# Performance work log

Hardware: AMD Instinct MI355X
Metric: run time of the kernel (lower is better)

Reference implementation:

```python
import jax, jax.numpy as jnp
import numpy as np

B, T, N, F_, KH, D, KD = 16, 12, 325, 64, 4, 16, 3  # batch, time, nodes, feat, heads, head_dim, diffusion steps
H = KH // 2
EPS = 1e-5


def setup_inputs() -> dict:
    key = jax.random.key(0)
    ks = jax.random.split(key, 16)
    lin = lambda k: (jax.random.normal(k, (F_, F_), jnp.float32) * 0.02)
    return {
        "x": jax.random.normal(ks[0], (B, T, N, F_), jnp.float32),
        "A": jax.random.uniform(ks[1], (KD, N, N), jnp.float32),
        "AT": jax.random.uniform(ks[2], (KD, N, N), jnp.float32),
        "Wq": lin(ks[3]), "bq": jnp.zeros((F_,), jnp.float32),
        "Wk": lin(ks[4]), "bk": jnp.zeros((F_,), jnp.float32),
        "Wks": lin(ks[5]), "bks": jnp.zeros((F_,), jnp.float32),
        "Wv": lin(ks[6]), "bv": jnp.zeros((F_,), jnp.float32),
        "Wvs": lin(ks[7]), "bvs": jnp.zeros((F_,), jnp.float32),
        "Wdi": jax.random.normal(ks[8], (H, KD, N, N), jnp.float32) * 0.05,
        "Wdo": jax.random.normal(ks[9], (H, KD, N, N), jnp.float32) * 0.05,
        "Wf1": lin(ks[10]), "bf1": jnp.zeros((F_,), jnp.float32),
        "Wf2": lin(ks[11]), "bf2": jnp.zeros((F_,), jnp.float32),
        "g_ln": jnp.ones((F_,), jnp.float32), "b_ln": jnp.zeros((F_,), jnp.float32),
    }


def _heads(y):
    # [B,T,N,F] -> [KH,B,T,N,D]  (torch.split along -1 then stack on dim 0)
    return y.reshape(B, T, N, KH, D).transpose(3, 0, 1, 2, 4)


def _attn_half(q, k, ks_, v, vs, bias):
    # q,k,ks_,v,vs: [H,B,T,N,D]; bias: [H,1,1,N,N]
    scale = 1.0 / jnp.sqrt(jnp.float32(D))
    e = jnp.einsum('hbtnd,hbtmd->hbtnm', q, k) * scale + bias
    es = jax.nn.sigmoid((q * ks_).sum(-1, keepdims=True) * scale)  # [H,B,T,N,1]
    e = e - e.max(-1, keepdims=True)
    ex = jnp.exp(e)
    a = ex / (es + ex.sum(-1, keepdims=True))  # sigmoid-augmented softmax
    out = jnp.einsum('hbtnm,hbtmd->hbtnd', a, v)
    return out + vs - a.sum(-1, keepdims=True) * vs


def reference(x, A, AT, Wq, bq, Wk, bk, Wks, bks, Wv, bv, Wvs, bvs,
              Wdi, Wdo, Wf1, bf1, Wf2, bf2, g_ln, b_ln):
    q = _heads(x @ Wq.T + bq)
    k = _heads(x @ Wk.T + bk)
    ks_ = _heads(x @ Wks.T + bks)
    v = _heads(x @ Wv.T + bv)
    vs = _heads(x @ Wvs.T + bvs)

    # DCN graph-diffusion bias: sum_j W[h,j] * A[j] -> [H,1,1,N,N]
    bias_i = jnp.einsum('hknm,knm->hnm', Wdi, A)[:, None, None]
    bias_o = jnp.einsum('hknm,knm->hnm', Wdo, AT)[:, None, None]

    vi = _attn_half(q[:H], k[:H], ks_[:H], v[:H], vs[:H], bias_i)
    vo = _attn_half(q[H:], k[H:], ks_[H:], v[H:], vs[H:], bias_o)

    val = jnp.concatenate([vi, vo], 0)  # [KH,B,T,N,D]
    val = val.transpose(1, 2, 3, 0, 4).reshape(B, T, N, F_)

    h = jax.nn.gelu(val @ Wf1.T + bf1, approximate=False) @ Wf2.T + bf2
    h = h + x

    mu = h.mean(-1, keepdims=True)
    var = ((h - mu) ** 2).mean(-1, keepdims=True)
    return g_ln * (h - mu) / jnp.sqrt(var + EPS) + b_ln
```

## Files before the change

kernel.cpp:

```cpp
#include <hip/hip_runtime.h>
#include <hip/hip_bf16.h>
#include <math.h>

#define NN 325
#define FD 64
#define KH 4
#define DH 16
#define BT 192
#define NN2 (NN*NN)
#define PST (NN*DH)
#define WSL 5632
#define HSTR 72
#define NPROJ 975
#define NBIAS 1848
#define NPAD  (KH*BT)
#define ANB   2112
#define LOG2E 1.44269504088896f

typedef __attribute__((ext_vector_type(8))) short short8;
typedef __attribute__((ext_vector_type(4))) float f32x4;

union U8 { uint4 u; short8 s; ushort us[8]; };
__device__ inline short8 lds8(const ushort* p){ U8 t; t.u = *(const uint4*)p; return t.s; }
__device__ inline float b2f(ushort v){ return __uint_as_float(((unsigned)v) << 16); }
__device__ inline ushort f2b(float f){
  unsigned u = __float_as_uint(f);
  u += 0x7fff + ((u >> 16) & 1);
  return (ushort)(u >> 16);
}
__device__ inline unsigned pk2(float a, float b){
  union { __hip_bfloat162 h; unsigned u; } t;
  t.h = __float22bfloat162_rn(float2{a, b});
  return t.u;
}
__device__ inline short8 cvt8(const float* p){
  float4 u = ((const float4*)p)[0], v = ((const float4*)p)[1];
  U8 t;
  t.us[0]=f2b(u.x); t.us[1]=f2b(u.y); t.us[2]=f2b(u.z); t.us[3]=f2b(u.w);
  t.us[4]=f2b(v.x); t.us[5]=f2b(v.y); t.us[6]=f2b(v.z); t.us[7]=f2b(v.w);
  return t.s;
}

__global__ __launch_bounds__(256) void wpack_kernel(
    const float* __restrict__ Wq,  const float* __restrict__ bq,
    const float* __restrict__ Wk,  const float* __restrict__ bk,
    const float* __restrict__ Wks, const float* __restrict__ bks,
    const float* __restrict__ Wv,  const float* __restrict__ bv,
    const float* __restrict__ Wvs, const float* __restrict__ bvs,
    const float* __restrict__ Wf1, const float* __restrict__ Wf2,
    ushort* __restrict__ Wcat, float* __restrict__ bcat){
  int blk = blockIdx.x;
  const float* Ws[7] = {Wq, Wk, Wks, Wv, Wvs, Wf1, Wf2};
  const float* bs[5] = {bq, bk, bks, bv, bvs};
  int f = blk * 64 + (threadIdx.x >> 2);
  int c0 = (threadIdx.x & 3) * 8;
  const float* wr = Ws[blk] + (f & 63) * 64;
  unsigned* dst = (unsigned*)Wcat + f * 32 + c0;
  #pragma unroll
  for (int c = 0; c < 8; ++c)
    dst[c] = f2b(wr[2*(c0+c)]) | ((unsigned)f2b(wr[2*(c0+c)+1]) << 16);
  if (blk < 5 && (threadIdx.x & 3) == 0) bcat[f] = bs[blk][f & 63];
}

__global__ __launch_bounds__(256) void prep_kernel(
    const float* __restrict__ x, const ushort* __restrict__ Wcat,
    const float* __restrict__ bcat, ushort* __restrict__ proj,
    ushort* __restrict__ vt, ushort* __restrict__ kperm,
    const float* __restrict__ Wdi, const float* __restrict__ Wdo,
    const float* __restrict__ A,   const float* __restrict__ AT,
    float* __restrict__ biasF){
  int bid = blockIdx.x, tid = threadIdx.x;
  if (bid < NPROJ){
    int lane = tid & 63, wid = tid >> 6;
    int r0 = bid * 64 + wid * 16;
    int m = lane & 15, g = lane >> 4;
    int gr = r0 + m;
    int bt = gr / NN, n = gr - bt * NN;
    const float* xr = x + (size_t)gr * 64 + g * 8;
    short8 xb0 = cvt8(xr);
    short8 xb1 = cvt8(xr + 32);
    for (int ct = 0; ct < 20; ++ct){
      short8 w0 = lds8(Wcat + ((size_t)(ct*16 + m) * 64 + g * 8));
      short8 w1 = lds8(Wcat + ((size_t)(ct*16 + m) * 64 + g * 8 + 32));
      float4 b4 = *(const float4*)(bcat + ct*16 + 4*g);
      f32x4 acc = {b4.x, b4.y, b4.z, b4.w};
      acc = __builtin_amdgcn_mfma_f32_16x16x32_bf16(w0, xb0, acc, 0, 0, 0);
      acc = __builtin_amdgcn_mfma_f32_16x16x32_bf16(w1, xb1, acc, 0, 0, 0);
      if (ct >= 4 && ct < 8){
        int w = n & 31;
        ushort* kd = kperm + (size_t)((ct-4)*BT + bt) * WSL
                   + (n >> 5)*512 + ((w >> 2) & 1)*256
                   + (4*(w >> 3) + (w & 3))*16 + 4*g;
        uint2 wv; wv.x = pk2(acc[0], acc[1]); wv.y = pk2(acc[2], acc[3]);
        *(uint2*)kd = wv;
      } else if (ct >= 12 && ct < 16){
        ushort* vs = vt + (size_t)((ct-12)*BT + bt) * WSL + (n >> 5)*512 + (n & 31);
        #pragma unroll
        for (int rg = 0; rg < 4; ++rg)
          vs[(4*g + rg) * 32] = f2b(acc[rg]);
      } else {
        int slot = (ct < 4) ? ct : (ct < 12 ? ct - 4 : ct - 8);
        float sc = (ct < 4) ? 0.25f * LOG2E : 1.0f;
        uint2 w2;
        w2.x = pk2(acc[0]*sc, acc[1]*sc);
        w2.y = pk2(acc[2]*sc, acc[3]*sc);
        *(uint2*)(proj + ((size_t)slot * BT + bt) * PST + n*16 + 4*g) = w2;
      }
    }
  } else if (bid < NPROJ + NBIAS){
    int idx = (bid - NPROJ) * 256 + tid;
    int h = idx / 118272;
    int rem = idx - h * 118272;
    int qt = rem / 5632;
    int r2 = rem - qt * 5632;
    int tt = r2 >> 9, r3 = r2 & 511;
    int gg = r3 >> 7, mm = (r3 >> 3) & 15, e8 = r3 & 7;
    int n = qt*16 + mm;
    int tok = tt*32 + gg*8 + e8;
    float s = -1e30f;
    if (n < NN && tok < NN){
      int ridx = n * NN + tok;
      s = 0.f;
      if (h < 2){
        #pragma unroll
        for (int k = 0; k < 3; ++k) s += Wdi[(h*3 + k)*NN2 + ridx] * A[k*NN2 + ridx];
      } else {
        int h2 = h - 2;
        #pragma unroll
        for (int k = 0; k < 3; ++k) s += Wdo[(h2*3 + k)*NN2 + ridx] * AT[k*NN2 + ridx];
      }
      s *= LOG2E;
    }
    biasF[idx] = s;
  } else {
    int slice = bid - NPROJ - NBIAS;
    if (tid < 432){
      int d = tid / 27, wz = 5 + tid % 27;
      vt[(size_t)slice * WSL + 5120 + d*32 + wz] = 0;
      int half = (wz >> 2) & 1, rr = 4*(wz >> 3) + (wz & 3);
      kperm[(size_t)slice * WSL + 5120 + half*256 + rr*16 + d] = 0;
    }
  }
}

__global__ __launch_bounds__(256, 3) void attn_kernel(
    const ushort* __restrict__ proj, const float* __restrict__ biasF,
    const ushort* __restrict__ vt, const ushort* __restrict__ kperm,
    ushort* __restrict__ val){
  int tid = threadIdx.x, lane = tid & 63, wid = tid >> 6;
  int bid = (int)blockIdx.x;
  int swz = (bid & 7) * (ANB/8) + (bid >> 3);
  int p = swz * 4 + wid;
  int j = p % 11, bh = p / 11;
  int h = bh / BT, bt = bh - h * BT;
  int qt1 = 2*j;
  int two = (j < 10);
  int qt2 = two ? qt1 + 1 : qt1;
  int m = lane & 15, g = lane >> 4;

  const ushort* qb  = proj + (size_t)((0*KH + h)*BT + bt) * PST;
  const ushort* ksb = proj + (size_t)((1*KH + h)*BT + bt) * PST;
  const ushort* vsb = proj + (size_t)((2*KH + h)*BT + bt) * PST;
  const ushort* ka  = kperm + (size_t)(h*BT + bt) * WSL + m*16 + (g&1)*8;
  const ushort* va  = vt    + (size_t)(h*BT + bt) * WSL + m*32 + g*8;
  const float*  b1a = biasF + (size_t)(h*21 + qt1) * WSL + g*128 + m*8;
  const float*  b2a = biasF + (size_t)(h*21 + qt2) * WSL + g*128 + m*8;

  short8 zero = {0,0,0,0,0,0,0,0};
  short8 qf1 = (g < 2) ? lds8(qb + (size_t)(qt1*16 + m)*16 + (g&1)*8) : zero;
  short8 qf2 = (g < 2) ? lds8(qb + (size_t)(qt2*16 + m)*16 + (g&1)*8) : zero;

  int nb1 = min(qt1*16 + m, NN-1), nb2 = min(qt2*16 + m, NN-1);
  uint2 qw1 = *(const uint2*)(qb  + (size_t)nb1*16 + g*4);
  uint2 kw1 = *(const uint2*)(ksb + (size_t)nb1*16 + g*4);
  uint2 qw2 = *(const uint2*)(qb  + (size_t)nb2*16 + g*4);
  uint2 kw2 = *(const uint2*)(ksb + (size_t)nb2*16 + g*4);

  short8 kE = lds8(ka), kO = lds8(ka + 256), vv = lds8(va);
  f32x4 bE1 = *(const f32x4*)(b1a), bO1 = *(const f32x4*)(b1a + 4);
  f32x4 bE2 = *(const f32x4*)(b2a), bO2 = *(const f32x4*)(b2a + 4);

  short8 ones = {16256,16256,16256,16256,16256,16256,16256,16256};
  f32x4 o1 = {0.f,0.f,0.f,0.f}, o2 = {0.f,0.f,0.f,0.f};
  f32x4 r1 = {0.f,0.f,0.f,0.f}, r2 = {0.f,0.f,0.f,0.f};

  #pragma unroll
  for (int tt = 0; tt < 11; ++tt){
    short8 kEn = zero, kOn = zero, vvn = zero;
    f32x4 bE1n = bE1, bO1n = bO1, bE2n = bE2, bO2n = bO2;
    if (tt < 10){
      const ushort* kan = ka + (tt+1)*512;
      kEn  = lds8(kan); kOn = lds8(kan + 256);
      vvn  = lds8(va + (tt+1)*512);
      bE1n = *(const f32x4*)(b1a + (tt+1)*512);
      bO1n = *(const f32x4*)(b1a + (tt+1)*512 + 4);
      bE2n = *(const f32x4*)(b2a + (tt+1)*512);
      bO2n = *(const f32x4*)(b2a + (tt+1)*512 + 4);
    }
    f32x4 aE1 = __builtin_amdgcn_mfma_f32_16x16x32_bf16(kE, qf1, bE1, 0, 0, 0);
    f32x4 aO1 = __builtin_amdgcn_mfma_f32_16x16x32_bf16(kO, qf1, bO1, 0, 0, 0);
    float e0 = __builtin_amdgcn_exp2f(aE1[0]);
    float e1 = __builtin_amdgcn_exp2f(aE1[1]);
    float e2 = __builtin_amdgcn_exp2f(aE1[2]);
    float e3 = __builtin_amdgcn_exp2f(aE1[3]);
    float e4 = __builtin_amdgcn_exp2f(aO1[0]);
    float e5 = __builtin_amdgcn_exp2f(aO1[1]);
    float e6 = __builtin_amdgcn_exp2f(aO1[2]);
    float e7 = __builtin_amdgcn_exp2f(aO1[3]);
    U8 p1;
    p1.u.x = pk2(e0, e1); p1.u.y = pk2(e2, e3);
    p1.u.z = pk2(e4, e5); p1.u.w = pk2(e6, e7);
    o1 = __builtin_amdgcn_mfma_f32_16x16x32_bf16(p1.s, vv,   o1, 0, 0, 0);
    r1 = __builtin_amdgcn_mfma_f32_16x16x32_bf16(p1.s, ones, r1, 0, 0, 0);
    f32x4 aE2 = __builtin_amdgcn_mfma_f32_16x16x32_bf16(kE, qf2, bE2, 0, 0, 0);
    f32x4 aO2 = __builtin_amdgcn_mfma_f32_16x16x32_bf16(kO, qf2, bO2, 0, 0, 0);
    float f0 = __builtin_amdgcn_exp2f(aE2[0]);
    float f1 = __builtin_amdgcn_exp2f(aE2[1]);
    float f2 = __builtin_amdgcn_exp2f(aE2[2]);
    float f3 = __builtin_amdgcn_exp2f(aE2[3]);
    float f4 = __builtin_amdgcn_exp2f(aO2[0]);
    float f5 = __builtin_amdgcn_exp2f(aO2[1]);
    float f6 = __builtin_amdgcn_exp2f(aO2[2]);
    float f7 = __builtin_amdgcn_exp2f(aO2[3]);
    U8 p2;
    p2.u.x = pk2(f0, f1); p2.u.y = pk2(f2, f3);
    p2.u.z = pk2(f4, f5); p2.u.w = pk2(f6, f7);
    o2 = __builtin_amdgcn_mfma_f32_16x16x32_bf16(p2.s, vv,   o2, 0, 0, 0);
    r2 = __builtin_amdgcn_mfma_f32_16x16x32_bf16(p2.s, ones, r2, 0, 0, 0);
    kE = kEn; kO = kOn; vv = vvn;
    bE1 = bE1n; bO1 = bO1n; bE2 = bE2n; bO2 = bO2n;
  }

  float dp1 = b2f((ushort)(qw1.x & 0xffff)) * b2f((ushort)(kw1.x & 0xffff))
            + b2f((ushort)(qw1.x >> 16))    * b2f((ushort)(kw1.x >> 16))
            + b2f((ushort)(qw1.y & 0xffff)) * b2f((ushort)(kw1.y & 0xffff))
            + b2f((ushort)(qw1.y >> 16))    * b2f((ushort)(kw1.y >> 16));
  float dp2 = b2f((ushort)(qw2.x & 0xffff)) * b2f((ushort)(kw2.x & 0xffff))
            + b2f((ushort)(qw2.x >> 16))    * b2f((ushort)(kw2.x >> 16))
            + b2f((ushort)(qw2.y & 0xffff)) * b2f((ushort)(kw2.y & 0xffff))
            + b2f((ushort)(qw2.y >> 16))    * b2f((ushort)(kw2.y >> 16));
  dp1 += __shfl_xor(dp1, 16, 64); dp1 += __shfl_xor(dp1, 32, 64);
  dp2 += __shfl_xor(dp2, 16, 64); dp2 += __shfl_xor(dp2, 32, 64);
  int sb = g << 4;
  #pragma unroll
  for (int rg = 0; rg < 4; ++rg){
    float d1 = __uint_as_float(__builtin_amdgcn_ds_bpermute(sb + rg*4, __float_as_uint(dp1)));
    float d2 = __uint_as_float(__builtin_amdgcn_ds_bpermute(sb + rg*4, __float_as_uint(dp2)));
    float es1 = __builtin_amdgcn_rcpf(1.f + __builtin_amdgcn_exp2f(-d1));
    float es2 = __builtin_amdgcn_rcpf(1.f + __builtin_amdgcn_exp2f(-d2));
    int n1 = qt1*16 + 4*g + rg;
    int n2 = qt2*16 + 4*g + rg;
    float vsx1 = b2f(vsb[(size_t)min(n1, NN-1)*16 + m]);
    float vsx2 = b2f(vsb[(size_t)min(n2, NN-1)*16 + m]);
    float iv1 = __builtin_amdgcn_rcpf(es1 + r1[rg]);
    float res1 = (o1[rg] + es1 * vsx1) * iv1;
    if (n1 < NN) val[((size_t)bt*NN + n1)*FD + h*16 + m] = f2b(res1);
    if (two){
      float iv2 = __builtin_amdgcn_rcpf(es2 + r2[rg]);
      float res2 = (o2[rg] + es2 * vsx2) * iv2;
      if (n2 < NN) val[((size_t)bt*NN + n2)*FD + h*16 + m] = f2b(res2);
    }
  }
}

__global__ __launch_bounds__(256) void ffn_kernel(
    const ushort* __restrict__ val, const float* __restrict__ x,
    const ushort* __restrict__ Wf1b, const float* __restrict__ bf1,
    const ushort* __restrict__ Wf2b, const float* __restrict__ bf2,
    const float* __restrict__ g_ln, const float* __restrict__ b_ln,
    float* __restrict__ out){
  __shared__ ushort hs[4][16 * HSTR];
  int tid = threadIdx.x, lane = tid & 63, wid = tid >> 6;
  int m = lane & 15, g = lane >> 4;
  int r0 = blockIdx.x * 64 + wid * 16;
  int row = r0 + m;

  short8 vb0 = lds8(val + ((size_t)row * 64 + g * 8));
  short8 vb1 = lds8(val + ((size_t)row * 64 + g * 8 + 32));

  #pragma unroll
  for (int ct = 0; ct < 4; ++ct){
    short8 w0 = lds8(Wf1b + ((size_t)(ct*16 + m) * 64 + g * 8));
    short8 w1 = lds8(Wf1b + ((size_t)(ct*16 + m) * 64 + g * 8 + 32));
    float4 b4 = *(const float4*)(bf1 + ct*16 + 4*g);
    f32x4 acc = {b4.x, b4.y, b4.z, b4.w};
    acc = __builtin_amdgcn_mfma_f32_16x16x32_bf16(w0, vb0, acc, 0, 0, 0);
    acc = __builtin_amdgcn_mfma_f32_16x16x32_bf16(w1, vb1, acc, 0, 0, 0);
    uint2 w;
    float g0 = 0.5f*acc[0]*(1.f + erff(acc[0]*0.70710678118654752f));
    float g1 = 0.5f*acc[1]*(1.f + erff(acc[1]*0.70710678118654752f));
    float g2 = 0.5f*acc[2]*(1.f + erff(acc[2]*0.70710678118654752f));
    float g3 = 0.5f*acc[3]*(1.f + erff(acc[3]*0.70710678118654752f));
    w.x = pk2(g0, g1); w.y = pk2(g2, g3);
    *(uint2*)&hs[wid][m * HSTR + ct*16 + 4*g] = w;
  }
  asm volatile("s_waitcnt lgkmcnt(0)" ::: "memory");
  short8 h0 = lds8(&hs[wid][m * HSTR + g * 8]);
  short8 h1 = lds8(&hs[wid][m * HSTR + g * 8 + 32]);

  float t[4][4];
  #pragma unroll
  for (int ct = 0; ct < 4; ++ct){
    short8 w0 = lds8(Wf2b + ((size_t)(ct*16 + m) * 64 + g * 8));
    short8 w1 = lds8(Wf2b + ((size_t)(ct*16 + m) * 64 + g * 8 + 32));
    float4 b4 = *(const float4*)(bf2 + ct*16 + 4*g);
    f32x4 acc = {b4.x, b4.y, b4.z, b4.w};
    acc = __builtin_amdgcn_mfma_f32_16x16x32_bf16(w0, h0, acc, 0, 0, 0);
    acc = __builtin_amdgcn_mfma_f32_16x16x32_bf16(w1, h1, acc, 0, 0, 0);
    float4 xr = *(const float4*)(x + (size_t)row * 64 + ct*16 + 4*g);
    t[ct][0] = acc[0] + xr.x; t[ct][1] = acc[1] + xr.y;
    t[ct][2] = acc[2] + xr.z; t[ct][3] = acc[3] + xr.w;
  }
  float s = 0.f;
  #pragma unroll
  for (int ct = 0; ct < 4; ++ct) s += (t[ct][0]+t[ct][1]) + (t[ct][2]+t[ct][3]);
  s += __shfl_xor(s, 16, 64); s += __shfl_xor(s, 32, 64);
  float mu = s * (1.f/64.f);
  float v = 0.f;
  #pragma unroll
  for (int ct = 0; ct < 4; ++ct){
    #pragma unroll
    for (int rg = 0; rg < 4; ++rg){ float d = t[ct][rg] - mu; v += d*d; }
  }
  v += __shfl_xor(v, 16, 64); v += __shfl_xor(v, 32, 64);
  float rs = rsqrtf(v * (1.f/64.f) + 1e-5f);
  #pragma unroll
  for (int ct = 0; ct < 4; ++ct){
    float4 g4 = *(const float4*)(g_ln + ct*16 + 4*g);
    float4 bb = *(const float4*)(b_ln + ct*16 + 4*g);
    float4 o;
    o.x = g4.x*(t[ct][0]-mu)*rs + bb.x;
    o.y = g4.y*(t[ct][1]-mu)*rs + bb.y;
    o.z = g4.z*(t[ct][2]-mu)*rs + bb.z;
    o.w = g4.w*(t[ct][3]-mu)*rs + bb.w;
    *(float4*)(out + (size_t)row * 64 + ct*16 + 4*g) = o;
  }
}

extern "C" void kernel_launch(void* const* d_in, const int* in_sizes, int n_in,
                              void* d_out, int out_size, void* d_ws, size_t ws_size,
                              hipStream_t stream) {
  const float* x    = (const float*)d_in[0];
  const float* A    = (const float*)d_in[1];
  const float* AT   = (const float*)d_in[2];
  const float* Wq   = (const float*)d_in[3];
  const float* bq   = (const float*)d_in[4];
  const float* Wk   = (const float*)d_in[5];
  const float* bk   = (const float*)d_in[6];
  const float* Wks  = (const float*)d_in[7];
  const float* bks  = (const float*)d_in[8];
  const float* Wv   = (const float*)d_in[9];
  const float* bv   = (const float*)d_in[10];
  const float* Wvs  = (const float*)d_in[11];
  const float* bvs  = (const float*)d_in[12];
  const float* Wdi  = (const float*)d_in[13];
  const float* Wdo  = (const float*)d_in[14];
  const float* Wf1  = (const float*)d_in[15];
  const float* bf1  = (const float*)d_in[16];
  const float* Wf2  = (const float*)d_in[17];
  const float* bf2  = (const float*)d_in[18];
  const float* g_ln = (const float*)d_in[19];
  const float* b_ln = (const float*)d_in[20];
  float* out = (float*)d_out;

  float* ws = (float*)d_ws;
  ushort* proj  = (ushort*)ws;
  float*  biasF = ws + 5990400;
  ushort* val   = (ushort*)(ws + 6463488);
  ushort* vt    = (ushort*)(ws + 8460288);
  ushort* kperm = (ushort*)(ws + 10622976);
  ushort* Wcat  = (ushort*)(ws + 12785664);
  float*  bcat  = ws + 12800000;
  ushort* Wf1b  = Wcat + 320*64;
  ushort* Wf2b  = Wcat + 384*64;

  wpack_kernel<<<7, 256, 0, stream>>>(Wq, bq, Wk, bk, Wks, bks,
                                      Wv, bv, Wvs, bvs, Wf1, Wf2, Wcat, bcat);
  prep_kernel<<<NPROJ + NBIAS + NPAD, 256, 0, stream>>>(
      x, Wcat, bcat, proj, vt, kperm, Wdi, Wdo, A, AT, biasF);
  attn_kernel<<<ANB, 256, 0, stream>>>(proj, biasF, vt, kperm, val);
  ffn_kernel<<<975, 256, 0, stream>>>(val, x, Wf1b, bf1, Wf2b, bf2,
                                      g_ln, b_ln, out);
}
```

Baseline: 188.6 us.

## Stage per-(head,bt) K and V slices in LDS shared across waves

Each attention block now handles one half of the query tiles for a single (head, batch-time) pair. It copies the permuted K and transposed V slices into shared memory once, and all waves then read them from LDS instead of each wave streaming them from global memory. The grid shrinks from 2112 to 1536 blocks and the occupancy hint of 3 blocks per CU is dropped. The costs are an LDS staging step plus a barrier, about 22 KB of LDS per block, and some idle waves: the first half has 6 tiles over 4 waves and the second has 5. The software prefetch of K/V across iterations is also removed.

```diff
diff --git a/kernel.cpp b/kernel.cpp
--- a/kernel.cpp
+++ b/kernel.cpp
@@ -14,7 +14,7 @@
 #define NPROJ 975
 #define NBIAS 1848
 #define NPAD  (KH*BT)
-#define ANB   2112
+#define ANB   1536
 #define LOG2E 1.44269504088896f
 
 typedef __attribute__((ext_vector_type(8))) short short8;
@@ -143,122 +143,137 @@
   }
 }
 
-__global__ __launch_bounds__(256, 3) void attn_kernel(
+__global__ __launch_bounds__(256) void attn_kernel(
     const ushort* __restrict__ proj, const float* __restrict__ biasF,
     const ushort* __restrict__ vt, const ushort* __restrict__ kperm,
     ushort* __restrict__ val){
+  __shared__ __align__(16) ushort Ks[WSL];
+  __shared__ __align__(16) ushort Vs[WSL];
   int tid = threadIdx.x, lane = tid & 63, wid = tid >> 6;
   int bid = (int)blockIdx.x;
-  int swz = (bid & 7) * (ANB/8) + (bid >> 3);
-  int p = swz * 4 + wid;
-  int j = p % 11, bh = p / 11;
-  int h = bh / BT, bt = bh - h * BT;
-  int qt1 = 2*j;
-  int two = (j < 10);
-  int qt2 = two ? qt1 + 1 : qt1;
+  int sub = bid & 1, pr = bid >> 1;
+  int h = pr / BT, bt = pr - h * BT;
   int m = lane & 15, g = lane >> 4;
 
   const ushort* qb  = proj + (size_t)((0*KH + h)*BT + bt) * PST;
   const ushort* ksb = proj + (size_t)((1*KH + h)*BT + bt) * PST;
   const ushort* vsb = proj + (size_t)((2*KH + h)*BT + bt) * PST;
-  const ushort* ka  = kperm + (size_t)(h*BT + bt) * WSL + m*16 + (g&1)*8;
-  const ushort* va  = vt    + (size_t)(h*BT + bt) * WSL + m*32 + g*8;
-  const float*  b1a = biasF + (size_t)(h*21 + qt1) * WSL + g*128 + m*8;
-  const float*  b2a = biasF + (size_t)(h*21 + qt2) * WSL + g*128 + m*8;
+  const ushort* kpb = kperm + (size_t)(h*BT + bt) * WSL;
+  const ushort* vtb = vt    + (size_t)(h*BT + bt) * WSL;
+
+  {
+    const uint4* ksrc = (const uint4*)kpb;
+    const uint4* vsrc = (const uint4*)vtb;
+    uint4* kdst = (uint4*)Ks;
+    uint4* vdst = (uint4*)Vs;
+    #pragma unroll
+    for (int i = 0; i < 3; ++i){
+      int idx = tid + i * 256;
+      if (idx < 704){ kdst[idx] = ksrc[idx]; vdst[idx] = vsrc[idx]; }
+    }
+  }
+  __syncthreads();
 
   short8 zero = {0,0,0,0,0,0,0,0};
-  short8 qf1 = (g < 2) ? lds8(qb + (size_t)(qt1*16 + m)*16 + (g&1)*8) : zero;
-  short8 qf2 = (g < 2) ? lds8(qb + (size_t)(qt2*16 + m)*16 + (g&1)*8) : zero;
-
-  int nb1 = min(qt1*16 + m, NN-1), nb2 = min(qt2*16 + m, NN-1);
-  uint2 qw1 = *(const uint2*)(qb  + (size_t)nb1*16 + g*4);
-  uint2 kw1 = *(const uint2*)(ksb + (size_t)nb1*16 + g*4);
-  uint2 qw2 = *(const uint2*)(qb  + (size_t)nb2*16 + g*4);
-  uint2 kw2 = *(const uint2*)(ksb + (size_t)nb2*16 + g*4);
-
-  short8 kE = lds8(ka), kO = lds8(ka + 256), vv = lds8(va);
-  f32x4 bE1 = *(const f32x4*)(b1a), bO1 = *(const f32x4*)(b1a + 4);
-  f32x4 bE2 = *(const f32x4*)(b2a), bO2 = *(const f32x4*)(b2a + 4);
-
   short8 ones = {16256,16256,16256,16256,16256,16256,16256,16256};
-  f32x4 o1 = {0.f,0.f,0.f,0.f}, o2 = {0.f,0.f,0.f,0.f};
-  f32x4 r1 = {0.f,0.f,0.f,0.f}, r2 = {0.f,0.f,0.f,0.f};
-
-  #pragma unroll
-  for (int tt = 0; tt < 11; ++tt){
-    short8 kEn = zero, kOn = zero, vvn = zero;
-    f32x4 bE1n = bE1, bO1n = bO1, bE2n = bE2, bO2n = bO2;
-    if (tt < 10){
-      const ushort* kan = ka + (tt+1)*512;
-      kEn  = lds8(kan); kOn = lds8(kan + 256);
-      vvn  = lds8(va + (tt+1)*512);
-      bE1n = *(const f32x4*)(b1a + (tt+1)*512);
-      bO1n = *(const f32x4*)(b1a + (tt+1)*512 + 4);
-      bE2n = *(const f32x4*)(b2a + (tt+1)*512);
-      bO2n = *(const f32x4*)(b2a + (tt+1)*512 + 4);
-    }
-    f32x4 aE1 = __builtin_amdgcn_mfma_f32_16x16x32_bf16(kE, qf1, bE1, 0, 0, 0);
-    f32x4 aO1 = __builtin_amdgcn_mfma_f32_16x16x32_bf16(kO, qf1, bO1, 0, 0, 0);
-    float e0 = __builtin_amdgcn_exp2f(aE1[0]);
-    float e1 = __builtin_amdgcn_exp2f(aE1[1]);
-    float e2 = __builtin_amdgcn_exp2f(aE1[2]);
-    float e3 = __builtin_amdgcn_exp2f(aE1[3]);
-    float e4 = __builtin_amdgcn_exp2f(aO1[0]);
-    float e5 = __builtin_amdgcn_exp2f(aO1[1]);
-    float e6 = __builtin_amdgcn_exp2f(aO1[2]);
-    float e7 = __builtin_amdgcn_exp2f(aO1[3]);
-    U8 p1;
-    p1.u.x = pk2(e0, e1); p1.u.y = pk2(e2, e3);
-    p1.u.z = pk2(e4, e5); p1.u.w = pk2(e6, e7);
-    o1 = __builtin_amdgcn_mfma_f32_16x16x32_bf16(p1.s, vv,   o1, 0, 0, 0);
-    r1 = __builtin_amdgcn_mfma_f32_16x16x32_bf16(p1.s, ones, r1, 0, 0, 0);
-    f32x4 aE2 = __builtin_amdgcn_mfma_f32_16x16x32_bf16(kE, qf2, bE2, 0, 0, 0);
-    f32x4 aO2 = __builtin_amdgcn_mfma_f32_16x16x32_bf16(kO, qf2, bO2, 0, 0, 0);
-    float f0 = __builtin_amdgcn_exp2f(aE2[0]);
-    float f1 = __builtin_amdgcn_exp2f(aE2[1]);
-    float f2 = __builtin_amdgcn_exp2f(aE2[2]);
-    float f3 = __builtin_amdgcn_exp2f(aE2[3]);
-    float f4 = __builtin_amdgcn_exp2f(aO2[0]);
-    float f5 = __builtin_amdgcn_exp2f(aO2[1]);
-    float f6 = __builtin_amdgcn_exp2f(aO2[2]);
-    float f7 = __builtin_amdgcn_exp2f(aO2[3]);
-    U8 p2;
-    p2.u.x = pk2(f0, f1); p2.u.y = pk2(f2, f3);
-    p2.u.z = pk2(f4, f5); p2.u.w = pk2(f6, f7);
-    o2 = __builtin_amdgcn_mfma_f32_16x16x32_bf16(p2.s, vv,   o2, 0, 0, 0);
-    r2 = __builtin_amdgcn_mfma_f32_16x16x32_bf16(p2.s, ones, r2, 0, 0, 0);
-    kE = kEn; kO = kOn; vv = vvn;
-    bE1 = bE1n; bO1 = bO1n; bE2 = bE2n; bO2 = bO2n;
-  }
-
-  float dp1 = b2f((ushort)(qw1.x & 0xffff)) * b2f((ushort)(kw1.x & 0xffff))
-            + b2f((ushort)(qw1.x >> 16))    * b2f((ushort)(kw1.x >> 16))
-            + b2f((ushort)(qw1.y & 0xffff)) * b2f((ushort)(kw1.y & 0xffff))
-            + b2f((ushort)(qw1.y >> 16))    * b2f((ushort)(kw1.y >> 16));
-  float dp2 = b2f((ushort)(qw2.x & 0xffff)) * b2f((ushort)(kw2.x & 0xffff))
-            + b2f((ushort)(qw2.x >> 16))    * b2f((ushort)(kw2.x >> 16))
-            + b2f((ushort)(qw2.y & 0xffff)) * b2f((ushort)(kw2.y & 0xffff))
-            + b2f((ushort)(qw2.y >> 16))    * b2f((ushort)(kw2.y >> 16));
-  dp1 += __shfl_xor(dp1, 16, 64); dp1 += __shfl_xor(dp1, 32, 64);
-  dp2 += __shfl_xor(dp2, 16, 64); dp2 += __shfl_xor(dp2, 32, 64);
-  int sb = g << 4;
-  #pragma unroll
-  for (int rg = 0; rg < 4; ++rg){
-    float d1 = __uint_as_float(__builtin_amdgcn_ds_bpermute(sb + rg*4, __float_as_uint(dp1)));
-    float d2 = __uint_as_float(__builtin_amdgcn_ds_bpermute(sb + rg*4, __float_as_uint(dp2)));
-    float es1 = __builtin_amdgcn_rcpf(1.f + __builtin_amdgcn_exp2f(-d1));
-    float es2 = __builtin_amdgcn_rcpf(1.f + __builtin_amdgcn_exp2f(-d2));
-    int n1 = qt1*16 + 4*g + rg;
-    int n2 = qt2*16 + 4*g + rg;
-    float vsx1 = b2f(vsb[(size_t)min(n1, NN-1)*16 + m]);
-    float vsx2 = b2f(vsb[(size_t)min(n2, NN-1)*16 + m]);
-    float iv1 = __builtin_amdgcn_rcpf(es1 + r1[rg]);
-    float res1 = (o1[rg] + es1 * vsx1) * iv1;
-    if (n1 < NN) val[((size_t)bt*NN + n1)*FD + h*16 + m] = f2b(res1);
-    if (two){
-      float iv2 = __builtin_amdgcn_rcpf(es2 + r2[rg]);
-      float res2 = (o2[rg] + es2 * vsx2) * iv2;
-      if (n2 < NN) val[((size_t)bt*NN + n2)*FD + h*16 + m] = f2b(res2);
+
+  int jend = sub ? 11 : 6;
+  for (int j = sub*6 + wid; j < jend; j += 4){
+    int qt1 = 2*j;
+    int two = (j < 10);
+    int qt2 = two ? qt1 + 1 : qt1;
+    const float* b1a = biasF + (size_t)(h*21 + qt1) * WSL + g*128 + m*8;
+    const float* b2a = biasF + (size_t)(h*21 + qt2) * WSL + g*128 + m*8;
+
+    short8 qf1 = (g < 2) ? lds8(qb + (size_t)(qt1*16 + m)*16 + (g&1)*8) : zero;
+    short8 qf2 = (g < 2) ? lds8(qb + (size_t)(qt2*16 + m)*16 + (g&1)*8) : zero;
+
+    int nb1 = min(qt1*16 + m, NN-1), nb2 = min(qt2*16 + m, NN-1);
+    uint2 qw1 = *(const uint2*)(qb  + (size_t)nb1*16 + g*4);
+    uint2 kw1 = *(const uint2*)(ksb + (size_t)nb1*16 + g*4);
+    uint2 qw2 = *(const uint2*)(qb  + (size_t)nb2*16 + g*4);
+    uint2 kw2 = *(const uint2*)(ksb + (size_t)nb2*16 + g*4);
+
+    f32x4 bE1 = *(const f32x4*)(b1a), bO1 = *(const f32x4*)(b1a + 4);
+    f32x4 bE2 = *(const f32x4*)(b2a), bO2 = *(const f32x4*)(b2a + 4);
+
+    f32x4 o1 = {0.f,0.f,0.f,0.f}, o2 = {0.f,0.f,0.f,0.f};
+    f32x4 r1 = {0.f,0.f,0.f,0.f}, r2 = {0.f,0.f,0.f,0.f};
+
+    #pragma unroll
+    for (int tt = 0; tt < 11; ++tt){
+      short8 kE = lds8(Ks + tt*512 + m*16 + (g&1)*8);
+      short8 kO = lds8(Ks + tt*512 + 256 + m*16 + (g&1)*8);
+      short8 vv = lds8(Vs + tt*512 + m*32 + g*8);
+      f32x4 bE1n = bE1, bO1n = bO1, bE2n = bE2, bO2n = bO2;
+      if (tt < 10){
+        bE1n = *(const f32x4*)(b1a + (tt+1)*512);
+        bO1n = *(const f32x4*)(b1a + (tt+1)*512 + 4);
+        bE2n = *(const f32x4*)(b2a + (tt+1)*512);
+        bO2n = *(const f32x4*)(b2a + (tt+1)*512 + 4);
+      }
+      f32x4 aE1 = __builtin_amdgcn_mfma_f32_16x16x32_bf16(kE, qf1, bE1, 0, 0, 0);
+      f32x4 aO1 = __builtin_amdgcn_mfma_f32_16x16x32_bf16(kO, qf1, bO1, 0, 0, 0);
+      float e0 = __builtin_amdgcn_exp2f(aE1[0]);
+      float e1 = __builtin_amdgcn_exp2f(aE1[1]);
+      float e2 = __builtin_amdgcn_exp2f(aE1[2]);
+      float e3 = __builtin_amdgcn_exp2f(aE1[3]);
+      float e4 = __builtin_amdgcn_exp2f(aO1[0]);
+      float e5 = __builtin_amdgcn_exp2f(aO1[1]);
+      float e6 = __builtin_amdgcn_exp2f(aO1[2]);
+      float e7 = __builtin_amdgcn_exp2f(aO1[3]);
+      U8 p1;
+      p1.u.x = pk2(e0, e1); p1.u.y = pk2(e2, e3);
+      p1.u.z = pk2(e4, e5); p1.u.w = pk2(e6, e7);
+      o1 = __builtin_amdgcn_mfma_f32_16x16x32_bf16(p1.s, vv,   o1, 0, 0, 0);
+      r1 = __builtin_amdgcn_mfma_f32_16x16x32_bf16(p1.s, ones, r1, 0, 0, 0);
+      f32x4 aE2 = __builtin_amdgcn_mfma_f32_16x16x32_bf16(kE, qf2, bE2, 0, 0, 0);
+      f32x4 aO2 = __builtin_amdgcn_mfma_f32_16x16x32_bf16(kO, qf2, bO2, 0, 0, 0);
+      float f0 = __builtin_amdgcn_exp2f(aE2[0]);
+      float f1 = __builtin_amdgcn_exp2f(aE2[1]);
+      float f2 = __builtin_amdgcn_exp2f(aE2[2]);
+      float f3 = __builtin_amdgcn_exp2f(aE2[3]);
+      float f4 = __builtin_amdgcn_exp2f(aO2[0]);
+      float f5 = __builtin_amdgcn_exp2f(aO2[1]);
+      float f6 = __builtin_amdgcn_exp2f(aO2[2]);
+      float f7 = __builtin_amdgcn_exp2f(aO2[3]);
+      U8 p2;
+      p2.u.x = pk2(f0, f1); p2.u.y = pk2(f2, f3);
+      p2.u.z = pk2(f4, f5); p2.u.w = pk2(f6, f7);
+      o2 = __builtin_amdgcn_mfma_f32_16x16x32_bf16(p2.s, vv,   o2, 0, 0, 0);
+      r2 = __builtin_amdgcn_mfma_f32_16x16x32_bf16(p2.s, ones, r2, 0, 0, 0);
+      bE1 = bE1n; bO1 = bO1n; bE2 = bE2n; bO2 = bO2n;
+    }
+
+    float dp1 = b2f((ushort)(qw1.x & 0xffff)) * b2f((ushort)(kw1.x & 0xffff))
+              + b2f((ushort)(qw1.x >> 16))    * b2f((ushort)(kw1.x >> 16))
+              + b2f((ushort)(qw1.y & 0xffff)) * b2f((ushort)(kw1.y & 0xffff))
+              + b2f((ushort)(qw1.y >> 16))    * b2f((ushort)(kw1.y >> 16));
+    float dp2 = b2f((ushort)(qw2.x & 0xffff)) * b2f((ushort)(kw2.x & 0xffff))
+              + b2f((ushort)(qw2.x >> 16))    * b2f((ushort)(kw2.x >> 16))
+              + b2f((ushort)(qw2.y & 0xffff)) * b2f((ushort)(kw2.y & 0xffff))
+              + b2f((ushort)(qw2.y >> 16))    * b2f((ushort)(kw2.y >> 16));
+    dp1 += __shfl_xor(dp1, 16, 64); dp1 += __shfl_xor(dp1, 32, 64);
+    dp2 += __shfl_xor(dp2, 16, 64); dp2 += __shfl_xor(dp2, 32, 64);
+    int sb = g << 4;
+    #pragma unroll
+    for (int rg = 0; rg < 4; ++rg){
+      float d1 = __uint_as_float(__builtin_amdgcn_ds_bpermute(sb + rg*4, __float_as_uint(dp1)));
+      float d2 = __uint_as_float(__builtin_amdgcn_ds_bpermute(sb + rg*4, __float_as_uint(dp2)));
+      float es1 = __builtin_amdgcn_rcpf(1.f + __builtin_amdgcn_exp2f(-d1));
+      float es2 = __builtin_amdgcn_rcpf(1.f + __builtin_amdgcn_exp2f(-d2));
+      int n1 = qt1*16 + 4*g + rg;
+      int n2 = qt2*16 + 4*g + rg;
+      float vsx1 = b2f(vsb[(size_t)min(n1, NN-1)*16 + m]);
+      float vsx2 = b2f(vsb[(size_t)min(n2, NN-1)*16 + m]);
+      float iv1 = __builtin_amdgcn_rcpf(es1 + r1[rg]);
+      float res1 = (o1[rg] + es1 * vsx1) * iv1;
+      if (n1 < NN) val[((size_t)bt*NN + n1)*FD + h*16 + m] = f2b(res1);
+      if (two){
+        float iv2 = __builtin_amdgcn_rcpf(es2 + r2[rg]);
+        float res2 = (o2[rg] + es2 * vsx2) * iv2;
+        if (n2 < NN) val[((size_t)bt*NN + n2)*FD + h*16 + m] = f2b(res2);
+      }
     }
   }
 }
```

Measured after the change: 213.2 us. 13.1% more time.
